# Performance work log

Measured on AMD Instinct MI355X. Metric: run time of the kernel, lower is better.

## Reference

```python
import jax, jax.numpy as jnp
from jax import lax
import numpy as np
import itertools

R = 7            # resolution
N = R * R        # 49 tokens
H = 8            # num_heads
KD = 32          # key_dim
QKD = 2 * H * KD # 512
VD = 2 * KD * H  # 512 (attn_ratio * key_dim * num_heads)
DIM = 384
B = 2048
SCALE = KD ** (-0.5)
BN_EPS = 1e-5


def _bias_idxs():
    points = list(itertools.product(range(R), range(R)))
    offsets = {}
    idxs = []
    for p1 in points:
        for p2 in points:
            o = (abs(p1[0] - p2[0]), abs(p1[1] - p2[1]))
            if o not in offsets:
                offsets[o] = len(offsets)
            idxs.append(offsets[o])
    return np.asarray(idxs, dtype=np.int32).reshape(N, N)  # [49,49], values in [0,49)


def setup_inputs() -> dict:
    key = jax.random.key(0)
    ks = jax.random.split(key, 8)
    return {
        "x": jax.random.normal(ks[0], (B, N, DIM), jnp.float32),
        "pwconv_w": jax.random.normal(ks[1], (QKD + VD, DIM), jnp.float32) * 0.05,
        "pwconv_b": jax.random.normal(ks[2], (QKD + VD,), jnp.float32) * 0.05,
        "dw_w": jax.random.normal(ks[3], (VD, 1, 3, 3), jnp.float32) * 0.1,
        "bn_gamma": jnp.ones((VD,), jnp.float32),
        "bn_beta": jnp.zeros((VD,), jnp.float32),
        "bn_mean": jnp.zeros((VD,), jnp.float32),
        "bn_var": jnp.ones((VD,), jnp.float32),
        "attn_biases": jax.random.normal(ks[4], (H, 49), jnp.float32) * 0.02,
        "proj_w": jax.random.normal(ks[5], (DIM, VD), jnp.float32) * 0.05,
        "proj_b": jnp.zeros((DIM,), jnp.float32),
        "bias_idxs": jnp.asarray(_bias_idxs()),
    }


def reference(x, pwconv_w, pwconv_b, dw_w, bn_gamma, bn_beta, bn_mean, bn_var,
              attn_biases, proj_w, proj_b, bias_idxs):
    b = x.shape[0]
    # [B,N,C] -> [B,C,7,7]
    xc = x.transpose(0, 2, 1).reshape(b, DIM, R, R)
    # 1x1 conv (pointwise) as einsum
    h = jnp.einsum('bchw,oc->bohw', xc, pwconv_w) + pwconv_b[None, :, None, None]
    qk, v1 = h[:, :QKD], h[:, QKD:]
    # [B,512,7,7] -> [B,2,H,KD,N] -> [2,B,H,N,KD]
    qk = qk.reshape(b, 2, H, KD, N).transpose(1, 0, 2, 4, 3)
    q, k = qk[0], qk[1]
    # depthwise 3x3 conv + BN (inference form) + exact GELU, residual into v1
    dw = lax.conv_general_dilated(v1, dw_w, (1, 1), 'SAME',
                                  feature_group_count=VD,
                                  dimension_numbers=('NCHW', 'OIHW', 'NCHW'))
    dw = (dw - bn_mean[None, :, None, None]) * (bn_gamma[None, :, None, None]
          * lax.rsqrt(bn_var[None, :, None, None] + BN_EPS)) + bn_beta[None, :, None, None]
    v1 = v1 + jax.nn.gelu(dw, approximate=False)
    # [B,VD,7,7] -> [B,H,dv,N] -> [B,H,N,dv]
    v = v1.reshape(b, H, VD // H, N).transpose(0, 1, 3, 2)
    bias = attn_biases[:, bias_idxs]  # [H,N,N] gathered relative-position bias
    attn = jax.nn.softmax(jnp.einsum('bhnd,bhmd->bhnm', q, k) * SCALE + bias[None], axis=-1)
    out = jnp.einsum('bhnm,bhmd->bhnd', attn, v).transpose(0, 2, 1, 3).reshape(b, N, VD)
    return out @ proj_w.T + proj_b
```

## Files before the change

### kernel.cpp

```cpp
#include <hip/hip_runtime.h>
#include <hip/hip_bf16.h>

#define NPOS 49
#define NH 8
#define DIMC 384
#define VDC 512
#define SCALE_QK 0.17677669529663687f

typedef unsigned short u16;
typedef __attribute__((ext_vector_type(8))) short bf16x8_t;
typedef __attribute__((ext_vector_type(4))) float f32x4_t;

__device__ __forceinline__ u16 f2bf(float f) {
    unsigned u = __float_as_uint(f);
    u = (u + 0x7fffu + ((u >> 16) & 1u)) >> 16;
    return (u16)u;
}
__device__ __forceinline__ float bf2f(u16 b) {
    return __uint_as_float(((unsigned)b) << 16);
}

__global__ __launch_bounds__(256) void prep_kernel(
    const float* __restrict__ pw, const float* __restrict__ pj,
    const float* __restrict__ ab, const int* __restrict__ bidx,
    u16* __restrict__ wpw, u16* __restrict__ wpj, float* __restrict__ biasf)
{
    int i = blockIdx.x * 256 + threadIdx.x;
    if (i < 1024 * 384) wpw[i] = f2bf(pw[i]);
    if (i < 384 * 512)  wpj[i] = f2bf(pj[i]);
    if (i < 8 * 49 * 49) {
        int h = i / (49 * 49);
        int nm = i - h * (49 * 49);
        biasf[i] = ab[h * 49 + bidx[nm]];
    }
}

__global__ __launch_bounds__(512) void fused_kernel(
    const float* __restrict__ x,
    const float* __restrict__ pwb,
    const float* __restrict__ dww,
    const float* __restrict__ bng, const float* __restrict__ bnb,
    const float* __restrict__ bnm, const float* __restrict__ bnv,
    const float* __restrict__ pjb,
    const u16* __restrict__ wpw, const u16* __restrict__ wpj,
    const float* __restrict__ biasf,
    float* __restrict__ out)
{
    __shared__ u16 lds[68224];
    const int tid  = threadIdx.x;
    const int b    = blockIdx.x;
    const int wv   = tid >> 6;
    const int lane = tid & 63;
    const int quad = lane >> 4;
    const int l16  = lane & 15;

    u16* s_x  = lds;
    u16* s_q  = lds;
    u16* s_k  = lds + 15680;
    u16* s_P  = lds;
    u16* s_v  = lds + 31360;
    u16* s_o2 = lds + 31360;

    const float* xb = x + (size_t)b * (NPOS * DIMC);
    for (int i = tid; i < NPOS * DIMC; i += 512) {
        int n = i / DIMC;
        int c = i - n * DIMC;
        s_x[n * 392 + c] = f2bf(xb[i]);
    }
    for (int i = tid; i < 512 * 23; i += 512) {
        int c = i / 23, j = i - c * 23;
        s_v[c * 72 + 49 + j] = 0;
    }
    __syncthreads();

    f32x4_t acc[8][4];
    #pragma unroll
    for (int nt = 0; nt < 8; ++nt)
        #pragma unroll
        for (int mt = 0; mt < 4; ++mt)
            acc[nt][mt] = (f32x4_t){0.f, 0.f, 0.f, 0.f};

    #pragma unroll
    for (int ks = 0; ks < 12; ++ks) {
        const int k0 = ks * 32 + quad * 8;
        bf16x8_t afr[4];
        #pragma unroll
        for (int mt = 0; mt < 4; ++mt)
            afr[mt] = *(const bf16x8_t*)(s_x + (mt * 16 + l16) * 392 + k0);
        #pragma unroll
        for (int nt = 0; nt < 8; ++nt) {
            const int och = wv * 128 + nt * 16 + l16;
            bf16x8_t bfr = *(const bf16x8_t*)(wpw + och * 384 + k0);
            #pragma unroll
            for (int mt = 0; mt < 4; ++mt)
                acc[nt][mt] = __builtin_amdgcn_mfma_f32_16x16x32_bf16(
                    afr[mt], bfr, acc[nt][mt], 0, 0, 0);
        }
    }
    __syncthreads();

    #pragma unroll
    for (int nt = 0; nt < 8; ++nt) {
        const int och = wv * 128 + nt * 16 + l16;
        const float bias = pwb[och];
        u16* dst;
        int stride;
        if (och < 256)      { dst = s_q + ((och >> 5) * 49) * 40 + (och & 31); stride = 40; }
        else if (och < 512) { int o2 = och - 256;
                              dst = s_k + ((o2 >> 5) * 49) * 40 + (o2 & 31); stride = 40; }
        else                { dst = s_v + (och - 512) * 72; stride = 1; }
        #pragma unroll
        for (int mt = 0; mt < 4; ++mt)
            #pragma unroll
            for (int r = 0; r < 4; ++r) {
                int pos = mt * 16 + quad * 4 + r;
                if (pos < 49) dst[pos * stride] = f2bf(acc[nt][mt][r] + bias);
            }
    }
    __syncthreads();

    {
        const int c = tid;
        u16* src = s_v + c * 72;
        float vv[49];
        #pragma unroll
        for (int i = 0; i < 49; ++i) vv[i] = bf2f(src[i]);
        float tap[9];
        #pragma unroll
        for (int j = 0; j < 9; ++j) tap[j] = dww[c * 9 + j];
        const float scale = bng[c] * rsqrtf(bnv[c] + 1e-5f);
        const float shift = bnb[c] - bnm[c] * scale;
        float res[49];
        #pragma unroll
        for (int y = 0; y < 7; ++y)
            #pragma unroll
            for (int xx = 0; xx < 7; ++xx) {
                float s = 0.f;
                #pragma unroll
                for (int ky = 0; ky < 3; ++ky)
                    #pragma unroll
                    for (int kx = 0; kx < 3; ++kx) {
                        int iy = y + ky - 1, ix = xx + kx - 1;
                        if (iy >= 0 && iy < 7 && ix >= 0 && ix < 7)
                            s += tap[ky * 3 + kx] * vv[iy * 7 + ix];
                    }
                s = s * scale + shift;
                float g = 0.5f * s * (1.0f + erff(s * 0.70710678118654752f));
                res[y * 7 + xx] = vv[y * 7 + xx] + g;
            }
        #pragma unroll
        for (int i = 0; i < 49; ++i) src[i] = f2bf(res[i]);
    }
    __syncthreads();

    {
        const int h = wv;
        bf16x8_t qa[4], kfr[4];
        #pragma unroll
        for (int mt = 0; mt < 4; ++mt)
            qa[mt] = *(const bf16x8_t*)(s_q + (h * 49 + mt * 16 + l16) * 40 + quad * 8);
        #pragma unroll
        for (int nt = 0; nt < 4; ++nt)
            kfr[nt] = *(const bf16x8_t*)(s_k + (h * 49 + nt * 16 + l16) * 40 + quad * 8);
        f32x4_t sc[4][4];
        #pragma unroll
        for (int mt = 0; mt < 4; ++mt)
            #pragma unroll
            for (int nt = 0; nt < 4; ++nt) {
                f32x4_t z = (f32x4_t){0.f, 0.f, 0.f, 0.f};
                sc[mt][nt] = __builtin_amdgcn_mfma_f32_16x16x32_bf16(qa[mt], kfr[nt], z, 0, 0, 0);
            }

        float pvreg[4][4][4];
        #pragma unroll
        for (int mt = 0; mt < 4; ++mt)
            #pragma unroll
            for (int r = 0; r < 4; ++r) {
                const int qrow = mt * 16 + quad * 4 + r;
                float sv[4];
                #pragma unroll
                for (int nt = 0; nt < 4; ++nt) {
                    const int key = nt * 16 + l16;
                    float val = sc[mt][nt][r] * SCALE_QK;
                    if (key < 49 && qrow < 49) val += biasf[(h * 49 + qrow) * 49 + key];
                    else                       val = -1e30f;
                    sv[nt] = val;
                }
                float mx = fmaxf(fmaxf(sv[0], sv[1]), fmaxf(sv[2], sv[3]));
                #pragma unroll
                for (int off = 1; off < 16; off <<= 1)
                    mx = fmaxf(mx, __shfl_xor(mx, off));
                float e0 = __expf(sv[0] - mx), e1 = __expf(sv[1] - mx);
                float e2 = __expf(sv[2] - mx), e3 = __expf(sv[3] - mx);
                float sum = e0 + e1 + e2 + e3;
                #pragma unroll
                for (int off = 1; off < 16; off <<= 1)
                    sum += __shfl_xor(sum, off);
                const float inv = 1.0f / sum;
                pvreg[mt][r][0] = e0 * inv; pvreg[mt][r][1] = e1 * inv;
                pvreg[mt][r][2] = e2 * inv; pvreg[mt][r][3] = e3 * inv;
            }
        __syncthreads();
        #pragma unroll
        for (int mt = 0; mt < 4; ++mt)
            #pragma unroll
            for (int r = 0; r < 4; ++r) {
                const int qrow = mt * 16 + quad * 4 + r;
                if (qrow < 49) {
                    #pragma unroll
                    for (int nt = 0; nt < 4; ++nt)
                        s_P[(h * 49 + qrow) * 72 + nt * 16 + l16] = f2bf(pvreg[mt][r][nt]);
                }
            }
        __syncthreads();

        f32x4_t oa[4][4];
        #pragma unroll
        for (int mt = 0; mt < 4; ++mt)
            #pragma unroll
            for (int nt = 0; nt < 4; ++nt)
                oa[mt][nt] = (f32x4_t){0.f, 0.f, 0.f, 0.f};
        #pragma unroll
        for (int ksv = 0; ksv < 2; ++ksv) {
            const int kb0 = ksv * 32 + quad * 8;
            bf16x8_t pa[4], vb[4];
            #pragma unroll
            for (int mt = 0; mt < 4; ++mt)
                pa[mt] = *(const bf16x8_t*)(s_P + (h * 49 + mt * 16 + l16) * 72 + kb0);
            #pragma unroll
            for (int nt = 0; nt < 4; ++nt)
                vb[nt] = *(const bf16x8_t*)(s_v + (h * 64 + nt * 16 + l16) * 72 + kb0);
            #pragma unroll
            for (int mt = 0; mt < 4; ++mt)
                #pragma unroll
                for (int nt = 0; nt < 4; ++nt)
                    oa[mt][nt] = __builtin_amdgcn_mfma_f32_16x16x32_bf16(
                        pa[mt], vb[nt], oa[mt][nt], 0, 0, 0);
        }
        __syncthreads();
        #pragma unroll
        for (int mt = 0; mt < 4; ++mt)
            #pragma unroll
            for (int nt = 0; nt < 4; ++nt)
                #pragma unroll
                for (int r = 0; r < 4; ++r) {
                    int pos = mt * 16 + quad * 4 + r;
                    if (pos < 49)
                        s_o2[pos * 520 + h * 64 + nt * 16 + l16] = f2bf(oa[mt][nt][r]);
                }
    }
    __syncthreads();

    {
        f32x4_t pacc[3][4];
        #pragma unroll
        for (int ntl = 0; ntl < 3; ++ntl)
            #pragma unroll
            for (int mt = 0; mt < 4; ++mt)
                pacc[ntl][mt] = (f32x4_t){0.f, 0.f, 0.f, 0.f};
        #pragma unroll
        for (int ks = 0; ks < 16; ++ks) {
            const int k0 = ks * 32 + quad * 8;
            bf16x8_t afr[4];
            #pragma unroll
            for (int mt = 0; mt < 4; ++mt)
                afr[mt] = *(const bf16x8_t*)(s_o2 + (mt * 16 + l16) * 520 + k0);
            #pragma unroll
            for (int ntl = 0; ntl < 3; ++ntl) {
                const int o = (wv * 3 + ntl) * 16 + l16;
                bf16x8_t wb = *(const bf16x8_t*)(wpj + o * 512 + k0);
                #pragma unroll
                for (int mt = 0; mt < 4; ++mt)
                    pacc[ntl][mt] = __builtin_amdgcn_mfma_f32_16x16x32_bf16(
                        afr[mt], wb, pacc[ntl][mt], 0, 0, 0);
            }
        }
        float* ob = out + (size_t)b * (NPOS * DIMC);
        #pragma unroll
        for (int ntl = 0; ntl < 3; ++ntl) {
            const int o = (wv * 3 + ntl) * 16 + l16;
            const float pb = pjb[o];
            #pragma unroll
            for (int mt = 0; mt < 4; ++mt)
                #pragma unroll
                for (int r = 0; r < 4; ++r) {
                    int pos = mt * 16 + quad * 4 + r;
                    if (pos < 49) ob[pos * 384 + o] = pacc[ntl][mt][r] + pb;
                }
        }
    }
}

extern "C" void kernel_launch(void* const* d_in, const int* in_sizes, int n_in,
                              void* d_out, int out_size, void* d_ws, size_t ws_size,
                              hipStream_t stream)
{
    const float* x   = (const float*)d_in[0];
    const float* pw  = (const float*)d_in[1];
    const float* pwb = (const float*)d_in[2];
    const float* dww = (const float*)d_in[3];
    const float* bng = (const float*)d_in[4];
    const float* bnb = (const float*)d_in[5];
    const float* bnm = (const float*)d_in[6];
    const float* bnv = (const float*)d_in[7];
    const float* ab  = (const float*)d_in[8];
    const float* pj  = (const float*)d_in[9];
    const float* pjb = (const float*)d_in[10];
    const int*  bidx = (const int*)d_in[11];
    float* out = (float*)d_out;

    u16* wpw   = (u16*)d_ws;
    u16* wpj   = wpw + 1024 * 384;
    float* bia = (float*)(wpj + 384 * 512);

    const int nb = in_sizes[0] / (NPOS * DIMC);

    prep_kernel<<<1536, 256, 0, stream>>>(pw, pj, ab, bidx, wpw, wpj, bia);
    fused_kernel<<<nb, 512, 0, stream>>>(x, pwb, dww, bng, bnb, bnm, bnv, pjb,
                                         wpw, wpj, bia, out);
}
```

Before: 716.2 us.

## Double block to 1024 threads and split per-stage work across sixteen waves

The fused kernel now launches with 1024 threads per block. Each stage's work is re-partitioned: half as many output tiles per wave in the pointwise GEMM, the depthwise conv split by row halves, attention split by query-tile halves per head, and projection tiles distributed as 24 over 16 waves. It also folds the QK scale into q at store time and vectorises the x load with float4. The aim is more waves per CU to hide latency, since the large LDS footprint limits occupancy to one block per CU. The cost is a 64-VGPR cap per thread, which could cause spills, plus an extra barrier and load imbalance in the projection stage.

```diff
diff --git a/kernel.cpp b/kernel.cpp
--- a/kernel.cpp
+++ b/kernel.cpp
@@ -35,7 +35,7 @@
     }
 }
 
-__global__ __launch_bounds__(512) void fused_kernel(
+__global__ __launch_bounds__(1024) void fused_kernel(
     const float* __restrict__ x,
     const float* __restrict__ pwb,
     const float* __restrict__ dww,
@@ -61,21 +61,23 @@
     u16* s_v  = lds + 31360;
     u16* s_o2 = lds + 31360;
 
-    const float* xb = x + (size_t)b * (NPOS * DIMC);
-    for (int i = tid; i < NPOS * DIMC; i += 512) {
-        int n = i / DIMC;
-        int c = i - n * DIMC;
-        s_x[n * 392 + c] = f2bf(xb[i]);
-    }
-    for (int i = tid; i < 512 * 23; i += 512) {
+    const float4* xb4 = (const float4*)(x + (size_t)b * (NPOS * DIMC));
+    for (int i = tid; i < (NPOS * DIMC) / 4; i += 1024) {
+        float4 t = xb4[i];
+        int n = i / 96;
+        int c = (i - n * 96) * 4;
+        u16* d = s_x + n * 392 + c;
+        d[0] = f2bf(t.x); d[1] = f2bf(t.y); d[2] = f2bf(t.z); d[3] = f2bf(t.w);
+    }
+    for (int i = tid; i < 512 * 23; i += 1024) {
         int c = i / 23, j = i - c * 23;
         s_v[c * 72 + 49 + j] = 0;
     }
     __syncthreads();
 
-    f32x4_t acc[8][4];
+    f32x4_t acc[4][4];
     #pragma unroll
-    for (int nt = 0; nt < 8; ++nt)
+    for (int nt = 0; nt < 4; ++nt)
         #pragma unroll
         for (int mt = 0; mt < 4; ++mt)
             acc[nt][mt] = (f32x4_t){0.f, 0.f, 0.f, 0.f};
@@ -88,8 +90,8 @@
         for (int mt = 0; mt < 4; ++mt)
             afr[mt] = *(const bf16x8_t*)(s_x + (mt * 16 + l16) * 392 + k0);
         #pragma unroll
-        for (int nt = 0; nt < 8; ++nt) {
-            const int och = wv * 128 + nt * 16 + l16;
+        for (int nt = 0; nt < 4; ++nt) {
+            const int och = wv * 64 + nt * 16 + l16;
             bf16x8_t bfr = *(const bf16x8_t*)(wpw + och * 384 + k0);
             #pragma unroll
             for (int mt = 0; mt < 4; ++mt)
@@ -100,9 +102,10 @@
     __syncthreads();
 
     #pragma unroll
-    for (int nt = 0; nt < 8; ++nt) {
-        const int och = wv * 128 + nt * 16 + l16;
+    for (int nt = 0; nt < 4; ++nt) {
+        const int och = wv * 64 + nt * 16 + l16;
         const float bias = pwb[och];
+        const float mul = (och < 256) ? SCALE_QK : 1.0f;
         u16* dst;
         int stride;
         if (och < 256)      { dst = s_q + ((och >> 5) * 49) * 40 + (och & 31); stride = 40; }
@@ -114,25 +117,33 @@
             #pragma unroll
             for (int r = 0; r < 4; ++r) {
                 int pos = mt * 16 + quad * 4 + r;
-                if (pos < 49) dst[pos * stride] = f2bf(acc[nt][mt][r] + bias);
+                if (pos < 49) dst[pos * stride] = f2bf((acc[nt][mt][r] + bias) * mul);
             }
     }
     __syncthreads();
 
     {
-        const int c = tid;
-        u16* src = s_v + c * 72;
-        float vv[49];
-        #pragma unroll
-        for (int i = 0; i < 49; ++i) vv[i] = bf2f(src[i]);
+        const int c    = tid & 511;
+        const int half = tid >> 9;
+        const int base = half * 16;
+        float vv[40];
+        #pragma unroll
+        for (int j = 0; j < 5; ++j) {
+            bf16x8_t raw = *(const bf16x8_t*)(s_v + c * 72 + base + 8 * j);
+            #pragma unroll
+            for (int e = 0; e < 8; ++e) vv[j * 8 + e] = bf2f(raw[e]);
+        }
         float tap[9];
         #pragma unroll
         for (int j = 0; j < 9; ++j) tap[j] = dww[c * 9 + j];
         const float scale = bng[c] * rsqrtf(bnv[c] + 1e-5f);
         const float shift = bnb[c] - bnm[c] * scale;
-        float res[49];
-        #pragma unroll
-        for (int y = 0; y < 7; ++y)
+        const int y0 = half ? 4 : 0;
+        const int ny = half ? 3 : 4;
+        float res[28];
+        for (int yy = 0; yy < 4; ++yy) {
+            if (yy >= ny) break;
+            const int y = y0 + yy;
             #pragma unroll
             for (int xx = 0; xx < 7; ++xx) {
                 float s = 0.f;
@@ -142,48 +153,58 @@
                     for (int kx = 0; kx < 3; ++kx) {
                         int iy = y + ky - 1, ix = xx + kx - 1;
                         if (iy >= 0 && iy < 7 && ix >= 0 && ix < 7)
-                            s += tap[ky * 3 + kx] * vv[iy * 7 + ix];
+                            s += tap[ky * 3 + kx] * vv[iy * 7 + ix - base];
                     }
                 s = s * scale + shift;
                 float g = 0.5f * s * (1.0f + erff(s * 0.70710678118654752f));
-                res[y * 7 + xx] = vv[y * 7 + xx] + g;
-            }
-        #pragma unroll
-        for (int i = 0; i < 49; ++i) src[i] = f2bf(res[i]);
+                res[yy * 7 + xx] = vv[y * 7 + xx - base] + g;
+            }
+        }
+        __syncthreads();
+        for (int yy = 0; yy < 4; ++yy) {
+            if (yy >= ny) break;
+            const int y = y0 + yy;
+            #pragma unroll
+            for (int xx = 0; xx < 7; ++xx)
+                s_v[c * 72 + y * 7 + xx] = f2bf(res[yy * 7 + xx]);
+        }
     }
     __syncthreads();
 
     {
-        const int h = wv;
-        bf16x8_t qa[4], kfr[4];
-        #pragma unroll
-        for (int mt = 0; mt < 4; ++mt)
-            qa[mt] = *(const bf16x8_t*)(s_q + (h * 49 + mt * 16 + l16) * 40 + quad * 8);
+        const int h    = wv >> 1;
+        const int half = wv & 1;
+        bf16x8_t qa[2], kfr[4];
+        #pragma unroll
+        for (int mtl = 0; mtl < 2; ++mtl)
+            qa[mtl] = *(const bf16x8_t*)(s_q + (h * 49 + (half * 2 + mtl) * 16 + l16) * 40 + quad * 8);
         #pragma unroll
         for (int nt = 0; nt < 4; ++nt)
             kfr[nt] = *(const bf16x8_t*)(s_k + (h * 49 + nt * 16 + l16) * 40 + quad * 8);
-        f32x4_t sc[4][4];
-        #pragma unroll
-        for (int mt = 0; mt < 4; ++mt)
+        f32x4_t sc[2][4];
+        #pragma unroll
+        for (int mtl = 0; mtl < 2; ++mtl)
             #pragma unroll
             for (int nt = 0; nt < 4; ++nt) {
                 f32x4_t z = (f32x4_t){0.f, 0.f, 0.f, 0.f};
-                sc[mt][nt] = __builtin_amdgcn_mfma_f32_16x16x32_bf16(qa[mt], kfr[nt], z, 0, 0, 0);
-            }
-
-        float pvreg[4][4][4];
-        #pragma unroll
-        for (int mt = 0; mt < 4; ++mt)
+                sc[mtl][nt] = __builtin_amdgcn_mfma_f32_16x16x32_bf16(qa[mtl], kfr[nt], z, 0, 0, 0);
+            }
+
+        float pvreg[2][4][4];
+        #pragma unroll
+        for (int mtl = 0; mtl < 2; ++mtl)
             #pragma unroll
             for (int r = 0; r < 4; ++r) {
-                const int qrow = mt * 16 + quad * 4 + r;
+                const int qrow = (half * 2 + mtl) * 16 + quad * 4 + r;
                 float sv[4];
                 #pragma unroll
                 for (int nt = 0; nt < 4; ++nt) {
                     const int key = nt * 16 + l16;
-                    float val = sc[mt][nt][r] * SCALE_QK;
-                    if (key < 49 && qrow < 49) val += biasf[(h * 49 + qrow) * 49 + key];
-                    else                       val = -1e30f;
+                    float val;
+                    if (key < 49 && qrow < 49)
+                        val = sc[mtl][nt][r] + biasf[(h * 49 + qrow) * 49 + key];
+                    else
+                        val = -1e30f;
                     sv[nt] = val;
                 }
                 float mx = fmaxf(fmaxf(sv[0], sv[1]), fmaxf(sv[2], sv[3]));
@@ -197,67 +218,70 @@
                 for (int off = 1; off < 16; off <<= 1)
                     sum += __shfl_xor(sum, off);
                 const float inv = 1.0f / sum;
-                pvreg[mt][r][0] = e0 * inv; pvreg[mt][r][1] = e1 * inv;
-                pvreg[mt][r][2] = e2 * inv; pvreg[mt][r][3] = e3 * inv;
+                pvreg[mtl][r][0] = e0 * inv; pvreg[mtl][r][1] = e1 * inv;
+                pvreg[mtl][r][2] = e2 * inv; pvreg[mtl][r][3] = e3 * inv;
             }
         __syncthreads();
         #pragma unroll
-        for (int mt = 0; mt < 4; ++mt)
+        for (int mtl = 0; mtl < 2; ++mtl)
             #pragma unroll
             for (int r = 0; r < 4; ++r) {
-                const int qrow = mt * 16 + quad * 4 + r;
+                const int qrow = (half * 2 + mtl) * 16 + quad * 4 + r;
                 if (qrow < 49) {
                     #pragma unroll
                     for (int nt = 0; nt < 4; ++nt)
-                        s_P[(h * 49 + qrow) * 72 + nt * 16 + l16] = f2bf(pvreg[mt][r][nt]);
+                        s_P[(h * 49 + qrow) * 72 + nt * 16 + l16] = f2bf(pvreg[mtl][r][nt]);
                 }
             }
         __syncthreads();
 
-        f32x4_t oa[4][4];
-        #pragma unroll
-        for (int mt = 0; mt < 4; ++mt)
+        f32x4_t oa[2][4];
+        #pragma unroll
+        for (int mtl = 0; mtl < 2; ++mtl)
             #pragma unroll
             for (int nt = 0; nt < 4; ++nt)
-                oa[mt][nt] = (f32x4_t){0.f, 0.f, 0.f, 0.f};
+                oa[mtl][nt] = (f32x4_t){0.f, 0.f, 0.f, 0.f};
         #pragma unroll
         for (int ksv = 0; ksv < 2; ++ksv) {
             const int kb0 = ksv * 32 + quad * 8;
-            bf16x8_t pa[4], vb[4];
-            #pragma unroll
-            for (int mt = 0; mt < 4; ++mt)
-                pa[mt] = *(const bf16x8_t*)(s_P + (h * 49 + mt * 16 + l16) * 72 + kb0);
+            bf16x8_t pa[2], vb[4];
+            #pragma unroll
+            for (int mtl = 0; mtl < 2; ++mtl)
+                pa[mtl] = *(const bf16x8_t*)(s_P + (h * 49 + (half * 2 + mtl) * 16 + l16) * 72 + kb0);
             #pragma unroll
             for (int nt = 0; nt < 4; ++nt)
                 vb[nt] = *(const bf16x8_t*)(s_v + (h * 64 + nt * 16 + l16) * 72 + kb0);
             #pragma unroll
-            for (int mt = 0; mt < 4; ++mt)
+            for (int mtl = 0; mtl < 2; ++mtl)
                 #pragma unroll
                 for (int nt = 0; nt < 4; ++nt)
-                    oa[mt][nt] = __builtin_amdgcn_mfma_f32_16x16x32_bf16(
-                        pa[mt], vb[nt], oa[mt][nt], 0, 0, 0);
+                    oa[mtl][nt] = __builtin_amdgcn_mfma_f32_16x16x32_bf16(
+                        pa[mtl], vb[nt], oa[mtl][nt], 0, 0, 0);
         }
         __syncthreads();
         #pragma unroll
-        for (int mt = 0; mt < 4; ++mt)
+        for (int mtl = 0; mtl < 2; ++mtl)
             #pragma unroll
             for (int nt = 0; nt < 4; ++nt)
                 #pragma unroll
                 for (int r = 0; r < 4; ++r) {
-                    int pos = mt * 16 + quad * 4 + r;
+                    int pos = (half * 2 + mtl) * 16 + quad * 4 + r;
                     if (pos < 49)
-                        s_o2[pos * 520 + h * 64 + nt * 16 + l16] = f2bf(oa[mt][nt][r]);
+                        s_o2[pos * 520 + h * 64 + nt * 16 + l16] = f2bf(oa[mtl][nt][r]);
                 }
     }
     __syncthreads();
 
     {
-        f32x4_t pacc[3][4];
-        #pragma unroll
-        for (int ntl = 0; ntl < 3; ++ntl)
-            #pragma unroll
-            for (int mt = 0; mt < 4; ++mt)
-                pacc[ntl][mt] = (f32x4_t){0.f, 0.f, 0.f, 0.f};
+        const int t1 = wv;
+        const int t2 = wv + 16;
+        const bool has2 = (t2 < 24);
+        f32x4_t pacc[2][4];
+        #pragma unroll
+        for (int tt = 0; tt < 2; ++tt)
+            #pragma unroll
+            for (int mt = 0; mt < 4; ++mt)
+                pacc[tt][mt] = (f32x4_t){0.f, 0.f, 0.f, 0.f};
         #pragma unroll
         for (int ks = 0; ks < 16; ++ks) {
             const int k0 = ks * 32 + quad * 8;
@@ -265,27 +289,31 @@
             #pragma unroll
             for (int mt = 0; mt < 4; ++mt)
                 afr[mt] = *(const bf16x8_t*)(s_o2 + (mt * 16 + l16) * 520 + k0);
-            #pragma unroll
-            for (int ntl = 0; ntl < 3; ++ntl) {
-                const int o = (wv * 3 + ntl) * 16 + l16;
-                bf16x8_t wb = *(const bf16x8_t*)(wpj + o * 512 + k0);
+            bf16x8_t wb1 = *(const bf16x8_t*)(wpj + (t1 * 16 + l16) * 512 + k0);
+            #pragma unroll
+            for (int mt = 0; mt < 4; ++mt)
+                pacc[0][mt] = __builtin_amdgcn_mfma_f32_16x16x32_bf16(
+                    afr[mt], wb1, pacc[0][mt], 0, 0, 0);
+            if (has2) {
+                bf16x8_t wb2 = *(const bf16x8_t*)(wpj + (t2 * 16 + l16) * 512 + k0);
                 #pragma unroll
                 for (int mt = 0; mt < 4; ++mt)
-                    pacc[ntl][mt] = __builtin_amdgcn_mfma_f32_16x16x32_bf16(
-                        afr[mt], wb, pacc[ntl][mt], 0, 0, 0);
+                    pacc[1][mt] = __builtin_amdgcn_mfma_f32_16x16x32_bf16(
+                        afr[mt], wb2, pacc[1][mt], 0, 0, 0);
             }
         }
         float* ob = out + (size_t)b * (NPOS * DIMC);
         #pragma unroll
-        for (int ntl = 0; ntl < 3; ++ntl) {
-            const int o = (wv * 3 + ntl) * 16 + l16;
+        for (int tt = 0; tt < 2; ++tt) {
+            if (tt == 1 && !has2) break;
+            const int o = (tt ? t2 : t1) * 16 + l16;
             const float pb = pjb[o];
             #pragma unroll
             for (int mt = 0; mt < 4; ++mt)
                 #pragma unroll
                 for (int r = 0; r < 4; ++r) {
                     int pos = mt * 16 + quad * 4 + r;
-                    if (pos < 49) ob[pos * 384 + o] = pacc[ntl][mt][r] + pb;
+                    if (pos < 49) ob[pos * 384 + o] = pacc[tt][mt][r] + pb;
                 }
         }
     }
@@ -316,6 +344,6 @@
     const int nb = in_sizes[0] / (NPOS * DIMC);
 
     prep_kernel<<<1536, 256, 0, stream>>>(pw, pj, ab, bidx, wpw, wpj, bia);
-    fused_kernel<<<nb, 512, 0, stream>>>(x, pwb, dww, bng, bnb, bnm, bnv, pjb,
-                                         wpw, wpj, bia, out);
-}
+    fused_kernel<<<nb, 1024, 0, stream>>>(x, pwb, dww, bng, bnb, bnm, bnv, pjb,
+                                          wpw, wpj, bia, out);
+}
```

Result: slower. 1.034 ms (+44.3%).
